# Kernel tuning notes

Measured on AMD Instinct MI355X. Metric: run time of the kernel, lower is better.

Reference implementation:

```python
import jax, jax.numpy as jnp
import numpy as np

SUB_NO = 20
T_NO = 201
E_NO = 2000
I_NO = 500
T_DATA = 20000

def _make_cden():
    C = np.zeros((SUB_NO, SUB_NO), dtype=np.float32)
    for i in range(SUB_NO):
        for c in (2 * i + 1, 2 * i + 2):
            if c < SUB_NO:
                C[i, c] = 1.0
    return C

C_DEN = _make_cden()
CHILDREN = [np.where(C_DEN[s] == 1)[0] for s in range(SUB_NO)]  # static tree structure


def setup_inputs() -> dict:
    key = jax.random.key(0)
    ks = jax.random.split(key, 12)
    eps = 1e-6
    inp = {}
    inp['S_e'] = jax.random.uniform(ks[0], (T_DATA, E_NO), dtype=jnp.float32)
    inp['S_i'] = jax.random.uniform(ks[1], (T_DATA, I_NO), dtype=jnp.float32)
    # uniform noise for REBAR reparam; clipped away from {0,1} so log(-log(u)) is finite
    inp['u'] = jnp.clip(jax.random.uniform(ks[2], (SUB_NO, E_NO + I_NO), dtype=jnp.float32), eps, 1.0 - eps)
    inp['v'] = jnp.clip(jax.random.uniform(ks[3], (SUB_NO, E_NO + I_NO), dtype=jnp.float32), eps, 1.0 - eps)
    inp['W_syn'] = jax.random.normal(ks[4], (SUB_NO, 2), dtype=jnp.float32) * 0.1
    inp['Tau_syn'] = jnp.ones((SUB_NO, 2), dtype=jnp.float32)
    inp['Delta_syn'] = jax.random.uniform(ks[5], (SUB_NO, 2), dtype=jnp.float32)
    inp['W_sub'] = jax.random.uniform(ks[6], (SUB_NO,), dtype=jnp.float32)
    inp['V_o'] = jax.random.normal(ks[7], (1,), dtype=jnp.float32)
    inp['Theta'] = jnp.zeros((SUB_NO,), dtype=jnp.float32)
    inp['C_syn_log'] = jnp.ones((SUB_NO, E_NO + I_NO), dtype=jnp.float32)
    return inp


def _H(x):
    # one-hot of per-column argmax (first max, as torch.argmax)
    idx = jnp.argmax(x, axis=0)
    return jax.nn.one_hot(idx, x.shape[0], axis=0, dtype=x.dtype)


def _reparam_pz(u, theta):
    return jnp.log(theta) - jnp.log(-jnp.log(u))


def _reparam_pz_b(v, b, theta):
    # b is one-hot per column; v_k = v at the b==1 row of each column
    v_k = jnp.sum(v * b, axis=0, keepdims=True)  # [1, cols]
    z_same = -jnp.log(-jnp.log(v))
    z_diff = -jnp.log(-jnp.log(v) / theta - jnp.log(v_k))
    return b * z_same + (1.0 - b) * z_diff


def _evaluate_f(C_syn, S_e, S_i, W_syn, Tau_syn, Delta_syn, W_sub, V_o):
    T_data = S_e.shape[0]
    C_syn_e = C_syn[:, :E_NO]          # [sub, E]
    C_syn_i = C_syn[:, -I_NO:]         # [sub, I]
    # double-exponential (alpha) synaptic kernels, vectorized over subunits & e/i
    t_raw = jnp.arange(T_NO, dtype=S_e.dtype)                               # [T_no]
    t = jnp.maximum(t_raw[None, None, :] - jnp.exp(Delta_syn)[:, :, None], 0.0)  # [sub,2,T_no]
    t_tau = t / jnp.exp(Tau_syn)[:, :, None]
    kern = t_tau * jnp.exp(-t_tau) * W_syn[:, :, None]                      # [sub,2,T_no]
    # project spikes onto subunits
    in_e = S_e @ C_syn_e.T   # [T, sub]
    in_i = S_i @ C_syn_i.T   # [T, sub]
    # causal depthwise conv: syn[t,s] = sum_tau kern[s,:,tau] * in[t-tau,s]
    inp = jnp.stack([in_e.T, in_i.T], axis=1).reshape(1, SUB_NO * 2, T_data)   # NCH
    k = jnp.flip(kern, axis=-1).reshape(SUB_NO * 2, 1, T_NO)                   # OIH
    filt = jax.lax.conv_general_dilated(
        inp, k, window_strides=(1,), padding=[(T_NO - 1, 0)],
        feature_group_count=SUB_NO * 2,
        dimension_numbers=('NCH', 'OIH', 'NCH'))
    syn_in = filt.reshape(SUB_NO, 2, T_data).sum(axis=1).T   # [T, sub]
    # tree-recurrent tanh aggregation (children have higher index than parents)
    sub_out = [None] * SUB_NO
    for s in range(SUB_NO):
        idx = SUB_NO - 1 - s
        ch = CHILDREN[idx]
        if ch.size == 0:
            sub_out[idx] = jnp.tanh(syn_in[:, idx])
        else:
            leaf = sum(sub_out[c] * W_sub[c] for c in ch)
            sub_out[idx] = jnp.tanh(syn_in[:, idx] + leaf)
    return sub_out[0] * W_sub[0] + V_o[0]


def reference(S_e, S_i, u, v, W_syn, Tau_syn, Delta_syn, W_sub, V_o, Theta, C_syn_log):
    theta = jax.nn.softmax(C_syn_log, axis=0)
    rebar_z = _reparam_pz(u, theta)
    hard_z = _H(rebar_z)
    rebar_zb = _reparam_pz_b(v, hard_z, theta)
    soft_z = jax.nn.sigmoid(rebar_z / 0.5) + 1e-9
    soft_zb = jax.nn.sigmoid(rebar_zb / 0.5) + 1e-9
    V_hard_z = _evaluate_f(hard_z, S_e, S_i, W_syn, Tau_syn, Delta_syn, W_sub, V_o)
    V_soft_z = _evaluate_f(soft_z, S_e, S_i, W_syn, Tau_syn, Delta_syn, W_sub, V_o)
    V_soft_zb = _evaluate_f(soft_zb, S_e, S_i, W_syn, Tau_syn, Delta_syn, W_sub, V_o)
    return (V_hard_z, V_soft_z, V_soft_zb, theta, hard_z, soft_z, soft_zb)
```

## Files before the change

kernel.cpp:

```cpp
#include <hip/hip_runtime.h>
#include <math.h>

#define SUBS 20
#define TAPS 201
#define ENO 2000
#define INO 500
#define TDATA 20000

typedef __bf16 bf16x8 __attribute__((ext_vector_type(8)));
typedef float f32x4 __attribute__((ext_vector_type(4)));

#define WGE_STRIDE 2048
#define WGI_STRIDE 512

#define WGE_OFF  0ull
#define WGI_OFF  262144ull
#define KERN_OFF 327680ull
#define INE_OFF  360448ull
#define INI_OFF  (INE_OFF + 4800000ull)
#define SYN_OFF  (INI_OFF + 4800000ull)

__device__ __forceinline__ unsigned short f2bf(float f) {
  union { float f; unsigned int u; } c; c.f = f;
  unsigned int u = c.u;
  return (unsigned short)((u + 0x7FFFu + ((u >> 16) & 1u)) >> 16);
}

__global__ __launch_bounds__(256) void prep_kernel(
    const float* __restrict__ u, const float* __restrict__ v,
    const float* __restrict__ C_log, const float* __restrict__ W_syn,
    const float* __restrict__ Tau_syn, const float* __restrict__ Delta_syn,
    float* __restrict__ out,
    unsigned short* __restrict__ wge, unsigned short* __restrict__ wgi,
    float* __restrict__ kern)
{
  if (blockIdx.x < 10) {
    const int n = blockIdx.x * 256 + threadIdx.x;
    if (n >= 2500) return;
    float x[SUBS], theta[SUBS], rebar[SUBS];
    float mx = -1e30f;
#pragma unroll
    for (int s = 0; s < SUBS; ++s) { x[s] = C_log[s*2500 + n]; mx = fmaxf(mx, x[s]); }
    float sum = 0.f;
#pragma unroll
    for (int s = 0; s < SUBS; ++s) { theta[s] = expf(x[s] - mx); sum += theta[s]; }
    const float inv = 1.f / sum;
    int idx = 0; float best = -1e30f;
#pragma unroll
    for (int s = 0; s < SUBS; ++s) {
      theta[s] *= inv;
      out[60000 + s*2500 + n] = theta[s];
      const float uu = u[s*2500 + n];
      const float r = logf(theta[s]) - logf(-logf(uu));
      rebar[s] = r;
      if (r > best) { best = r; idx = s; }
    }
    const float lvk = logf(v[idx*2500 + n]);
#pragma unroll
    for (int s = 0; s < SUBS; ++s) {
      const float hz = (s == idx) ? 1.f : 0.f;
      const float sz = 1.f / (1.f + expf(-2.f * rebar[s])) + 1e-9f;
      const float vv = v[s*2500 + n];
      const float zb = (s == idx) ? (-logf(-logf(vv)))
                                  : (-logf(-logf(vv) / theta[s] - lvk));
      const float szb = 1.f / (1.f + expf(-2.f * zb)) + 1e-9f;
      out[110000 + s*2500 + n] = hz;
      out[160000 + s*2500 + n] = sz;
      out[210000 + s*2500 + n] = szb;
      if (n < ENO) {
        wge[(s     )*WGE_STRIDE + n] = f2bf(hz);
        wge[(20 + s)*WGE_STRIDE + n] = f2bf(sz);
        wge[(40 + s)*WGE_STRIDE + n] = f2bf(szb);
      } else {
        const int k = n - ENO;
        wgi[(s     )*WGI_STRIDE + k] = f2bf(hz);
        wgi[(20 + s)*WGI_STRIDE + k] = f2bf(sz);
        wgi[(40 + s)*WGI_STRIDE + k] = f2bf(szb);
      }
    }
  } else {
    const int tid = threadIdx.x;
    for (int i = tid; i < 40*TAPS; i += 256) {
      const int ch = i / TAPS, m = i - ch*TAPS;
      const float dl  = expf(Delta_syn[ch]);
      const float tau = expf(Tau_syn[ch]);
      const float t  = fmaxf((float)m - dl, 0.f);
      const float tt = t / tau;
      kern[i] = tt * expf(-tt) * W_syn[ch];
    }
    for (int i = tid; i < 4*2048; i += 256) wge[(60 + (i >> 11))*WGE_STRIDE + (i & 2047)] = 0;
    for (int i = tid; i < 60*48;  i += 256) wge[(i / 48)*WGE_STRIDE + 2000 + (i % 48)] = 0;
    for (int i = tid; i < 4*512;  i += 256) wgi[(60 + (i >> 9))*WGI_STRIDE + (i & 511)] = 0;
    for (int i = tid; i < 60*12;  i += 256) wgi[(i / 12)*WGI_STRIDE + 500 + (i % 12)] = 0;
  }
}

__global__ __launch_bounds__(256) void gemm_kernel(
    const float* __restrict__ S_e, const float* __restrict__ S_i,
    const unsigned short* __restrict__ wge, const unsigned short* __restrict__ wgi,
    float* __restrict__ in_e, float* __restrict__ in_i)
{
  __shared__ unsigned short Alds[64*40];
  __shared__ unsigned short Blds[64*40];
  __shared__ float Cbuf[64*68];
  const int tid  = threadIdx.x;
  const int t0   = blockIdx.x * 64;
  const int wave = tid >> 6;
  const int lane = tid & 63;
  const int m16  = lane & 15;
  const int quad = lane >> 4;
  const int slotA = tid & 7;
  const int rowA  = tid >> 3;
  const int cB    = tid >> 2;
  const int slotB = tid & 3;

  for (int phase = 0; phase < 2; ++phase) {
    const float* S = phase ? S_i : S_e;
    const unsigned short* Wg = phase ? wgi : wge;
    float* outp = phase ? in_i : in_e;
    const int K       = phase ? INO : ENO;
    const int Wstride = phase ? WGI_STRIDE : WGE_STRIDE;
    const int steps   = phase ? 16 : 63;

    f32x4 acc0 = {0.f,0.f,0.f,0.f};
    f32x4 acc1 = acc0, acc2 = acc0, acc3 = acc0;

    for (int st = 0; st < steps; ++st) {
      const int k0 = st * 32;
#pragma unroll
      for (int p = 0; p < 2; ++p) {
        const int r = rowA + p*32;
        const int t = t0 + r;
        const int k = k0 + slotA*4;
        float4 val = make_float4(0.f, 0.f, 0.f, 0.f);
        if (t < TDATA) {
          if (k + 4 <= K) {
            val = *(const float4*)(S + (size_t)t*K + k);
          } else {
            val.x = (k+0 < K) ? S[(size_t)t*K + k+0] : 0.f;
            val.y = (k+1 < K) ? S[(size_t)t*K + k+1] : 0.f;
            val.z = (k+2 < K) ? S[(size_t)t*K + k+2] : 0.f;
            val.w = (k+3 < K) ? S[(size_t)t*K + k+3] : 0.f;
          }
        }
        unsigned short* dst = &Alds[r*40 + slotA*4];
        dst[0] = f2bf(val.x); dst[1] = f2bf(val.y);
        dst[2] = f2bf(val.z); dst[3] = f2bf(val.w);
      }
      *(uint4*)(&Blds[cB*40 + slotB*8]) =
          *(const uint4*)(Wg + (size_t)cB*Wstride + k0 + slotB*8);
      __syncthreads();
      const bf16x8 a  = *(const bf16x8*)(&Alds[(wave*16 + m16)*40 + quad*8]);
      const bf16x8 b0 = *(const bf16x8*)(&Blds[(      m16)*40 + quad*8]);
      const bf16x8 b1 = *(const bf16x8*)(&Blds[(16 + m16)*40 + quad*8]);
      const bf16x8 b2 = *(const bf16x8*)(&Blds[(32 + m16)*40 + quad*8]);
      const bf16x8 b3 = *(const bf16x8*)(&Blds[(48 + m16)*40 + quad*8]);
      acc0 = __builtin_amdgcn_mfma_f32_16x16x32_bf16(a, b0, acc0, 0, 0, 0);
      acc1 = __builtin_amdgcn_mfma_f32_16x16x32_bf16(a, b1, acc1, 0, 0, 0);
      acc2 = __builtin_amdgcn_mfma_f32_16x16x32_bf16(a, b2, acc2, 0, 0, 0);
      acc3 = __builtin_amdgcn_mfma_f32_16x16x32_bf16(a, b3, acc3, 0, 0, 0);
      __syncthreads();
    }
    const int rloc = wave*16 + quad*4;
#pragma unroll
    for (int r = 0; r < 4; ++r) {
      Cbuf[(      m16)*68 + rloc + r] = acc0[r];
      Cbuf[(16 + m16)*68 + rloc + r] = acc1[r];
      Cbuf[(32 + m16)*68 + rloc + r] = acc2[r];
      Cbuf[(48 + m16)*68 + rloc + r] = acc3[r];
    }
    __syncthreads();
    if (cB < 60) {
#pragma unroll
      for (int g = 0; g < 4; ++g) {
        const int tl = slotB*16 + g*4;
        const int t = t0 + tl;
        if (t < TDATA)
          *(float4*)(outp + (size_t)cB*TDATA + t) = *(const float4*)(&Cbuf[cB*68 + tl]);
      }
    }
    __syncthreads();
  }
}

__device__ __forceinline__ int swz(int i) { return i + (i >> 5); }

__global__ __launch_bounds__(256) void conv_kernel(
    const float* __restrict__ in_e, const float* __restrict__ in_i,
    const float* __restrict__ kern, float* __restrict__ syn)
{
  __shared__ float Ee[2320];
  __shared__ float Ei[2320];
  const int ch = blockIdx.y;
  const int t0 = blockIdx.x * 2048;
  const int s  = ch % SUBS;
  const float* pe = in_e + (size_t)ch * TDATA;
  const float* pi = in_i + (size_t)ch * TDATA;
  for (int i = threadIdx.x; i < 2248; i += 256) {
    const int g = t0 - 200 + i;
    const bool ok = (g >= 0) && (g < TDATA);
    Ee[swz(i)] = ok ? pe[g] : 0.f;
    Ei[swz(i)] = ok ? pi[g] : 0.f;
  }
  __syncthreads();
  const float* ke = kern + (size_t)(s*2    ) * TAPS;
  const float* ki = kern + (size_t)(s*2 + 1) * TAPS;
  const int tb = threadIdx.x * 8;
  float acc[8] = {0.f,0.f,0.f,0.f,0.f,0.f,0.f,0.f};
  float we[8], wi[8];
#pragma unroll
  for (int j = 0; j < 8; ++j) {
    we[j] = Ee[swz(tb + 200 + j)];
    wi[j] = Ei[swz(tb + 200 + j)];
  }
#pragma unroll 8
  for (int m = 0; m < TAPS; ++m) {
    const float k0 = ke[m];
    const float k1 = ki[m];
#pragma unroll
    for (int j = 0; j < 8; ++j)
      acc[j] = fmaf(we[j], k0, fmaf(wi[j], k1, acc[j]));
    if (m < TAPS - 1) {
#pragma unroll
      for (int j = 7; j > 0; --j) { we[j] = we[j-1]; wi[j] = wi[j-1]; }
      we[0] = Ee[swz(tb + 199 - m)];
      wi[0] = Ei[swz(tb + 199 - m)];
    }
  }
  const int t = t0 + tb;
  if (t < TDATA) {
    float* o = syn + (size_t)ch * TDATA + t;
    *(float4*)(o    ) = make_float4(acc[0], acc[1], acc[2], acc[3]);
    *(float4*)(o + 4) = make_float4(acc[4], acc[5], acc[6], acc[7]);
  }
}

__global__ __launch_bounds__(256) void tree_kernel(
    const float* __restrict__ syn, const float* __restrict__ W_sub,
    const float* __restrict__ V_o, float* __restrict__ out)
{
  const int t = blockIdx.x * 256 + threadIdx.x;
  const int var = blockIdx.y;
  if (t >= TDATA) return;
  const float* sp = syn + (size_t)var * SUBS * TDATA + t;
  float so[SUBS];
#pragma unroll
  for (int s = SUBS - 1; s >= 0; --s) {
    float val = sp[(size_t)s * TDATA];
    const int c1 = 2*s + 1, c2 = 2*s + 2;
    if (c1 < SUBS) val += so[c1] * W_sub[c1];
    if (c2 < SUBS) val += so[c2] * W_sub[c2];
    so[s] = tanhf(val);
  }
  out[(size_t)var * TDATA + t] = so[0] * W_sub[0] + V_o[0];
}

extern "C" void kernel_launch(void* const* d_in, const int* in_sizes, int n_in,
                              void* d_out, int out_size, void* d_ws, size_t ws_size,
                              hipStream_t stream) {
  const float* S_e     = (const float*)d_in[0];
  const float* S_i     = (const float*)d_in[1];
  const float* u       = (const float*)d_in[2];
  const float* v       = (const float*)d_in[3];
  const float* W_syn   = (const float*)d_in[4];
  const float* Tau_syn = (const float*)d_in[5];
  const float* Delta   = (const float*)d_in[6];
  const float* W_sub   = (const float*)d_in[7];
  const float* V_o     = (const float*)d_in[8];
  const float* C_log   = (const float*)d_in[10];
  float* out = (float*)d_out;
  char* ws = (char*)d_ws;
  unsigned short* wge = (unsigned short*)(ws + WGE_OFF);
  unsigned short* wgi = (unsigned short*)(ws + WGI_OFF);
  float* kern = (float*)(ws + KERN_OFF);
  float* in_e = (float*)(ws + INE_OFF);
  float* in_i = (float*)(ws + INI_OFF);
  float* syn  = (float*)(ws + SYN_OFF);

  prep_kernel<<<dim3(11), dim3(256), 0, stream>>>(u, v, C_log, W_syn, Tau_syn,
                                                  Delta, out, wge, wgi, kern);
  gemm_kernel<<<dim3(313), dim3(256), 0, stream>>>(S_e, S_i, wge, wgi, in_e, in_i);
  conv_kernel<<<dim3(10, 60), dim3(256), 0, stream>>>(in_e, in_i, kern, syn);
  tree_kernel<<<dim3(79, 3), dim3(256), 0, stream>>>(syn, W_sub, V_o, out);
}
```

Measured before the change: 397.1 us.

## Split GEMM K dimension across blocks with atomic accumulation for more parallelism

The GEMM grid grows from 313 blocks to 313x5: the E-phase K=2000 is split into four 512-wide chunks whose partial sums are combined with atomicAdd, and the I-phase runs as its own chunk. Before, each block ran both phases one after the other. The E output buffer is now zeroed by extra blocks in the prep kernel, and the A/B/C LDS tiles share one union. The aim is to fill the GPU's many CUs instead of running about one block per CU with a long serial K loop. The cost is 4x atomic traffic on in_e, a zeroing pass over 9.6 MB, scalar strided output stores, and non-deterministic float summation order.

Result: slower. 580.0 us (+46.1%).

```diff
diff --git a/kernel.cpp b/kernel.cpp
--- a/kernel.cpp
+++ b/kernel.cpp
@@ -20,6 +20,8 @@
 #define INI_OFF  (INE_OFF + 4800000ull)
 #define SYN_OFF  (INI_OFF + 4800000ull)
 
+#define ZERO_BLOCKS 117
+
 __device__ __forceinline__ unsigned short f2bf(float f) {
   union { float f; unsigned int u; } c; c.f = f;
   unsigned int u = c.u;
@@ -32,7 +34,7 @@
     const float* __restrict__ Tau_syn, const float* __restrict__ Delta_syn,
     float* __restrict__ out,
     unsigned short* __restrict__ wge, unsigned short* __restrict__ wgi,
-    float* __restrict__ kern)
+    float* __restrict__ kern, float* __restrict__ in_e)
 {
   if (blockIdx.x < 10) {
     const int n = blockIdx.x * 256 + threadIdx.x;
@@ -78,7 +80,7 @@
         wgi[(40 + s)*WGI_STRIDE + k] = f2bf(szb);
       }
     }
-  } else {
+  } else if (blockIdx.x == 10) {
     const int tid = threadIdx.x;
     for (int i = tid; i < 40*TAPS; i += 256) {
       const int ch = i / TAPS, m = i - ch*TAPS;
@@ -92,6 +94,12 @@
     for (int i = tid; i < 60*48;  i += 256) wge[(i / 48)*WGE_STRIDE + 2000 + (i % 48)] = 0;
     for (int i = tid; i < 4*512;  i += 256) wgi[(60 + (i >> 9))*WGI_STRIDE + (i & 511)] = 0;
     for (int i = tid; i < 60*12;  i += 256) wgi[(i / 12)*WGI_STRIDE + 500 + (i % 12)] = 0;
+  } else {
+    const int zb = blockIdx.x - 11;
+    const int total4 = (2 * 60 * TDATA) / 4;
+    const float4 z = make_float4(0.f, 0.f, 0.f, 0.f);
+    for (int i = zb*256 + threadIdx.x; i < total4; i += ZERO_BLOCKS*256)
+      ((float4*)in_e)[i] = z;
   }
 }
 
@@ -100,11 +108,14 @@
     const unsigned short* __restrict__ wge, const unsigned short* __restrict__ wgi,
     float* __restrict__ in_e, float* __restrict__ in_i)
 {
-  __shared__ unsigned short Alds[64*40];
-  __shared__ unsigned short Blds[64*40];
-  __shared__ float Cbuf[64*68];
+  __shared__ union {
+    struct { unsigned short A[64*40]; unsigned short B[64*40]; } s;
+    float C[64*67];
+  } lds;
   const int tid  = threadIdx.x;
   const int t0   = blockIdx.x * 64;
+  const int chunk = blockIdx.y;
+  const bool isE = (chunk < 4);
   const int wave = tid >> 6;
   const int lane = tid & 63;
   const int m16  = lane & 15;
@@ -114,72 +125,76 @@
   const int cB    = tid >> 2;
   const int slotB = tid & 3;
 
-  for (int phase = 0; phase < 2; ++phase) {
-    const float* S = phase ? S_i : S_e;
-    const unsigned short* Wg = phase ? wgi : wge;
-    float* outp = phase ? in_i : in_e;
-    const int K       = phase ? INO : ENO;
-    const int Wstride = phase ? WGI_STRIDE : WGE_STRIDE;
-    const int steps   = phase ? 16 : 63;
-
-    f32x4 acc0 = {0.f,0.f,0.f,0.f};
-    f32x4 acc1 = acc0, acc2 = acc0, acc3 = acc0;
-
-    for (int st = 0; st < steps; ++st) {
-      const int k0 = st * 32;
-#pragma unroll
-      for (int p = 0; p < 2; ++p) {
-        const int r = rowA + p*32;
-        const int t = t0 + r;
-        const int k = k0 + slotA*4;
-        float4 val = make_float4(0.f, 0.f, 0.f, 0.f);
-        if (t < TDATA) {
-          if (k + 4 <= K) {
-            val = *(const float4*)(S + (size_t)t*K + k);
-          } else {
-            val.x = (k+0 < K) ? S[(size_t)t*K + k+0] : 0.f;
-            val.y = (k+1 < K) ? S[(size_t)t*K + k+1] : 0.f;
-            val.z = (k+2 < K) ? S[(size_t)t*K + k+2] : 0.f;
-            val.w = (k+3 < K) ? S[(size_t)t*K + k+3] : 0.f;
-          }
+  const float* S = isE ? S_e : S_i;
+  const unsigned short* Wg = isE ? wgi : wgi;
+  Wg = isE ? wge : wgi;
+  float* outp = isE ? in_e : in_i;
+  const int K       = isE ? ENO : INO;
+  const int Wstride = isE ? WGE_STRIDE : WGI_STRIDE;
+  const int k_base  = isE ? chunk * 512 : 0;
+  const int steps   = (chunk == 3) ? 15 : 16;
+
+  f32x4 acc0 = {0.f,0.f,0.f,0.f};
+  f32x4 acc1 = acc0, acc2 = acc0, acc3 = acc0;
+
+  for (int st = 0; st < steps; ++st) {
+    const int k0 = k_base + st * 32;
+#pragma unroll
+    for (int p = 0; p < 2; ++p) {
+      const int r = rowA + p*32;
+      const int t = t0 + r;
+      const int k = k0 + slotA*4;
+      float4 val = make_float4(0.f, 0.f, 0.f, 0.f);
+      if (t < TDATA) {
+        if (k + 4 <= K) {
+          val = *(const float4*)(S + (size_t)t*K + k);
+        } else {
+          val.x = (k+0 < K) ? S[(size_t)t*K + k+0] : 0.f;
+          val.y = (k+1 < K) ? S[(size_t)t*K + k+1] : 0.f;
+          val.z = (k+2 < K) ? S[(size_t)t*K + k+2] : 0.f;
+          val.w = (k+3 < K) ? S[(size_t)t*K + k+3] : 0.f;
         }
-        unsigned short* dst = &Alds[r*40 + slotA*4];
-        dst[0] = f2bf(val.x); dst[1] = f2bf(val.y);
-        dst[2] = f2bf(val.z); dst[3] = f2bf(val.w);
       }
-      *(uint4*)(&Blds[cB*40 + slotB*8]) =
-          *(const uint4*)(Wg + (size_t)cB*Wstride + k0 + slotB*8);
-      __syncthreads();
-      const bf16x8 a  = *(const bf16x8*)(&Alds[(wave*16 + m16)*40 + quad*8]);
-      const bf16x8 b0 = *(const bf16x8*)(&Blds[(      m16)*40 + quad*8]);
-      const bf16x8 b1 = *(const bf16x8*)(&Blds[(16 + m16)*40 + quad*8]);
-      const bf16x8 b2 = *(const bf16x8*)(&Blds[(32 + m16)*40 + quad*8]);
-      const bf16x8 b3 = *(const bf16x8*)(&Blds[(48 + m16)*40 + quad*8]);
-      acc0 = __builtin_amdgcn_mfma_f32_16x16x32_bf16(a, b0, acc0, 0, 0, 0);
-      acc1 = __builtin_amdgcn_mfma_f32_16x16x32_bf16(a, b1, acc1, 0, 0, 0);
-      acc2 = __builtin_amdgcn_mfma_f32_16x16x32_bf16(a, b2, acc2, 0, 0, 0);
-      acc3 = __builtin_amdgcn_mfma_f32_16x16x32_bf16(a, b3, acc3, 0, 0, 0);
-      __syncthreads();
-    }
-    const int rloc = wave*16 + quad*4;
-#pragma unroll
-    for (int r = 0; r < 4; ++r) {
-      Cbuf[(      m16)*68 + rloc + r] = acc0[r];
-      Cbuf[(16 + m16)*68 + rloc + r] = acc1[r];
-      Cbuf[(32 + m16)*68 + rloc + r] = acc2[r];
-      Cbuf[(48 + m16)*68 + rloc + r] = acc3[r];
-    }
+      ushort4 w4;
+      w4.x = f2bf(val.x); w4.y = f2bf(val.y);
+      w4.z = f2bf(val.z); w4.w = f2bf(val.w);
+      *(ushort4*)(&lds.s.A[r*40 + slotA*4]) = w4;
+    }
+    *(uint4*)(&lds.s.B[cB*40 + slotB*8]) =
+        *(const uint4*)(Wg + (size_t)cB*Wstride + k0 + slotB*8);
     __syncthreads();
-    if (cB < 60) {
-#pragma unroll
-      for (int g = 0; g < 4; ++g) {
-        const int tl = slotB*16 + g*4;
-        const int t = t0 + tl;
-        if (t < TDATA)
-          *(float4*)(outp + (size_t)cB*TDATA + t) = *(const float4*)(&Cbuf[cB*68 + tl]);
+    const bf16x8 a  = *(const bf16x8*)(&lds.s.A[(wave*16 + m16)*40 + quad*8]);
+    const bf16x8 b0 = *(const bf16x8*)(&lds.s.B[(      m16)*40 + quad*8]);
+    const bf16x8 b1 = *(const bf16x8*)(&lds.s.B[(16 + m16)*40 + quad*8]);
+    const bf16x8 b2 = *(const bf16x8*)(&lds.s.B[(32 + m16)*40 + quad*8]);
+    const bf16x8 b3 = *(const bf16x8*)(&lds.s.B[(48 + m16)*40 + quad*8]);
+    acc0 = __builtin_amdgcn_mfma_f32_16x16x32_bf16(a, b0, acc0, 0, 0, 0);
+    acc1 = __builtin_amdgcn_mfma_f32_16x16x32_bf16(a, b1, acc1, 0, 0, 0);
+    acc2 = __builtin_amdgcn_mfma_f32_16x16x32_bf16(a, b2, acc2, 0, 0, 0);
+    acc3 = __builtin_amdgcn_mfma_f32_16x16x32_bf16(a, b3, acc3, 0, 0, 0);
+    __syncthreads();
+  }
+  const int rloc = wave*16 + quad*4;
+#pragma unroll
+  for (int r = 0; r < 4; ++r) {
+    lds.C[(      m16)*67 + rloc + r] = acc0[r];
+    lds.C[(16 + m16)*67 + rloc + r] = acc1[r];
+    lds.C[(32 + m16)*67 + rloc + r] = acc2[r];
+    lds.C[(48 + m16)*67 + rloc + r] = acc3[r];
+  }
+  __syncthreads();
+  if (cB < 60) {
+    float* o = outp + (size_t)cB * TDATA;
+#pragma unroll
+    for (int g = 0; g < 16; ++g) {
+      const int tl = slotB*16 + g;
+      const int t = t0 + tl;
+      if (t < TDATA) {
+        const float val = lds.C[cB*67 + tl];
+        if (isE) atomicAdd(o + t, val);
+        else     o[t] = val;
       }
     }
-    __syncthreads();
   }
 }
 
@@ -277,9 +292,9 @@
   float* in_i = (float*)(ws + INI_OFF);
   float* syn  = (float*)(ws + SYN_OFF);
 
-  prep_kernel<<<dim3(11), dim3(256), 0, stream>>>(u, v, C_log, W_syn, Tau_syn,
-                                                  Delta, out, wge, wgi, kern);
-  gemm_kernel<<<dim3(313), dim3(256), 0, stream>>>(S_e, S_i, wge, wgi, in_e, in_i);
+  prep_kernel<<<dim3(11 + ZERO_BLOCKS), dim3(256), 0, stream>>>(
+      u, v, C_log, W_syn, Tau_syn, Delta, out, wge, wgi, kern, in_e);
+  gemm_kernel<<<dim3(313, 5), dim3(256), 0, stream>>>(S_e, S_i, wge, wgi, in_e, in_i);
   conv_kernel<<<dim3(10, 60), dim3(256), 0, stream>>>(in_e, in_i, kern, syn);
   tree_kernel<<<dim3(79, 3), dim3(256), 0, stream>>>(syn, W_sub, V_o, out);
 }
```

## Split GEMM K dimension across a 2D grid and add partial-sum reduction

Applied to the files above, without the earlier changes.

The GEMM grid becomes (313,3): the excitatory K range is split across two chunks and the inhibitory input gets its own chunk, which raises the block count from 313 to 939 to improve CU occupancy on a 256-CU GPU. The second excitatory chunk writes partial sums into the syn workspace, and a new reduce kernel adds them into in_e before the convolution. Accumulators are now stored straight from MFMA registers to global memory instead of being transposed through an LDS C buffer. The A-tile LDS store is vectorized as a ushort4. The cost is an extra kernel launch plus an extra read/write pass over the 60xT partial buffer, and the direct stores are less coalesced.

Result: faster. 343.6 us (-13.5%).

```diff
diff --git a/kernel.cpp b/kernel.cpp
--- a/kernel.cpp
+++ b/kernel.cpp
@@ -98,13 +98,14 @@
 __global__ __launch_bounds__(256) void gemm_kernel(
     const float* __restrict__ S_e, const float* __restrict__ S_i,
     const unsigned short* __restrict__ wge, const unsigned short* __restrict__ wgi,
-    float* __restrict__ in_e, float* __restrict__ in_i)
+    float* __restrict__ in_e, float* __restrict__ in_i, float* __restrict__ part)
 {
   __shared__ unsigned short Alds[64*40];
   __shared__ unsigned short Blds[64*40];
-  __shared__ float Cbuf[64*68];
   const int tid  = threadIdx.x;
   const int t0   = blockIdx.x * 64;
+  const int chunk = blockIdx.y;
+  const bool isE = (chunk < 2);
   const int wave = tid >> 6;
   const int lane = tid & 63;
   const int m16  = lane & 15;
@@ -114,72 +115,75 @@
   const int cB    = tid >> 2;
   const int slotB = tid & 3;
 
-  for (int phase = 0; phase < 2; ++phase) {
-    const float* S = phase ? S_i : S_e;
-    const unsigned short* Wg = phase ? wgi : wge;
-    float* outp = phase ? in_i : in_e;
-    const int K       = phase ? INO : ENO;
-    const int Wstride = phase ? WGI_STRIDE : WGE_STRIDE;
-    const int steps   = phase ? 16 : 63;
-
-    f32x4 acc0 = {0.f,0.f,0.f,0.f};
-    f32x4 acc1 = acc0, acc2 = acc0, acc3 = acc0;
-
-    for (int st = 0; st < steps; ++st) {
-      const int k0 = st * 32;
-#pragma unroll
-      for (int p = 0; p < 2; ++p) {
-        const int r = rowA + p*32;
-        const int t = t0 + r;
-        const int k = k0 + slotA*4;
-        float4 val = make_float4(0.f, 0.f, 0.f, 0.f);
-        if (t < TDATA) {
-          if (k + 4 <= K) {
-            val = *(const float4*)(S + (size_t)t*K + k);
-          } else {
-            val.x = (k+0 < K) ? S[(size_t)t*K + k+0] : 0.f;
-            val.y = (k+1 < K) ? S[(size_t)t*K + k+1] : 0.f;
-            val.z = (k+2 < K) ? S[(size_t)t*K + k+2] : 0.f;
-            val.w = (k+3 < K) ? S[(size_t)t*K + k+3] : 0.f;
-          }
+  const float* S = isE ? S_e : S_i;
+  const unsigned short* Wg = isE ? wge : wgi;
+  float* outp = (chunk == 0) ? in_e : ((chunk == 1) ? part : in_i);
+  const int K       = isE ? ENO : INO;
+  const int Wstride = isE ? WGE_STRIDE : WGI_STRIDE;
+  const int k_base  = (chunk == 1) ? 1024 : 0;
+  const int steps   = (chunk == 0) ? 32 : ((chunk == 1) ? 31 : 16);
+
+  f32x4 acc0 = {0.f,0.f,0.f,0.f};
+  f32x4 acc1 = acc0, acc2 = acc0, acc3 = acc0;
+
+  for (int st = 0; st < steps; ++st) {
+    const int k0 = k_base + st * 32;
+#pragma unroll
+    for (int p = 0; p < 2; ++p) {
+      const int r = rowA + p*32;
+      const int t = t0 + r;
+      const int k = k0 + slotA*4;
+      float4 val = make_float4(0.f, 0.f, 0.f, 0.f);
+      if (t < TDATA) {
+        if (k + 4 <= K) {
+          val = *(const float4*)(S + (size_t)t*K + k);
+        } else {
+          val.x = (k+0 < K) ? S[(size_t)t*K + k+0] : 0.f;
+          val.y = (k+1 < K) ? S[(size_t)t*K + k+1] : 0.f;
+          val.z = (k+2 < K) ? S[(size_t)t*K + k+2] : 0.f;
+          val.w = (k+3 < K) ? S[(size_t)t*K + k+3] : 0.f;
         }
-        unsigned short* dst = &Alds[r*40 + slotA*4];
-        dst[0] = f2bf(val.x); dst[1] = f2bf(val.y);
-        dst[2] = f2bf(val.z); dst[3] = f2bf(val.w);
       }
-      *(uint4*)(&Blds[cB*40 + slotB*8]) =
-          *(const uint4*)(Wg + (size_t)cB*Wstride + k0 + slotB*8);
-      __syncthreads();
-      const bf16x8 a  = *(const bf16x8*)(&Alds[(wave*16 + m16)*40 + quad*8]);
-      const bf16x8 b0 = *(const bf16x8*)(&Blds[(      m16)*40 + quad*8]);
-      const bf16x8 b1 = *(const bf16x8*)(&Blds[(16 + m16)*40 + quad*8]);
-      const bf16x8 b2 = *(const bf16x8*)(&Blds[(32 + m16)*40 + quad*8]);
-      const bf16x8 b3 = *(const bf16x8*)(&Blds[(48 + m16)*40 + quad*8]);
-      acc0 = __builtin_amdgcn_mfma_f32_16x16x32_bf16(a, b0, acc0, 0, 0, 0);
-      acc1 = __builtin_amdgcn_mfma_f32_16x16x32_bf16(a, b1, acc1, 0, 0, 0);
-      acc2 = __builtin_amdgcn_mfma_f32_16x16x32_bf16(a, b2, acc2, 0, 0, 0);
-      acc3 = __builtin_amdgcn_mfma_f32_16x16x32_bf16(a, b3, acc3, 0, 0, 0);
-      __syncthreads();
-    }
-    const int rloc = wave*16 + quad*4;
-#pragma unroll
-    for (int r = 0; r < 4; ++r) {
-      Cbuf[(      m16)*68 + rloc + r] = acc0[r];
-      Cbuf[(16 + m16)*68 + rloc + r] = acc1[r];
-      Cbuf[(32 + m16)*68 + rloc + r] = acc2[r];
-      Cbuf[(48 + m16)*68 + rloc + r] = acc3[r];
-    }
+      ushort4 w4;
+      w4.x = f2bf(val.x); w4.y = f2bf(val.y);
+      w4.z = f2bf(val.z); w4.w = f2bf(val.w);
+      *(ushort4*)(&Alds[r*40 + slotA*4]) = w4;
+    }
+    *(uint4*)(&Blds[cB*40 + slotB*8]) =
+        *(const uint4*)(Wg + (size_t)cB*Wstride + k0 + slotB*8);
     __syncthreads();
-    if (cB < 60) {
-#pragma unroll
-      for (int g = 0; g < 4; ++g) {
-        const int tl = slotB*16 + g*4;
-        const int t = t0 + tl;
-        if (t < TDATA)
-          *(float4*)(outp + (size_t)cB*TDATA + t) = *(const float4*)(&Cbuf[cB*68 + tl]);
-      }
-    }
+    const bf16x8 a  = *(const bf16x8*)(&Alds[(wave*16 + m16)*40 + quad*8]);
+    const bf16x8 b0 = *(const bf16x8*)(&Blds[(      m16)*40 + quad*8]);
+    const bf16x8 b1 = *(const bf16x8*)(&Blds[(16 + m16)*40 + quad*8]);
+    const bf16x8 b2 = *(const bf16x8*)(&Blds[(32 + m16)*40 + quad*8]);
+    const bf16x8 b3 = *(const bf16x8*)(&Blds[(48 + m16)*40 + quad*8]);
+    acc0 = __builtin_amdgcn_mfma_f32_16x16x32_bf16(a, b0, acc0, 0, 0, 0);
+    acc1 = __builtin_amdgcn_mfma_f32_16x16x32_bf16(a, b1, acc1, 0, 0, 0);
+    acc2 = __builtin_amdgcn_mfma_f32_16x16x32_bf16(a, b2, acc2, 0, 0, 0);
+    acc3 = __builtin_amdgcn_mfma_f32_16x16x32_bf16(a, b3, acc3, 0, 0, 0);
     __syncthreads();
+  }
+  const int t = t0 + wave*16 + quad*4;
+  if (t < TDATA) {
+    float* o = outp + t;
+    *(float4*)(o + (size_t)(     m16)*TDATA) = *(float4*)&acc0;
+    *(float4*)(o + (size_t)(16 + m16)*TDATA) = *(float4*)&acc1;
+    *(float4*)(o + (size_t)(32 + m16)*TDATA) = *(float4*)&acc2;
+    if (m16 < 12)
+      *(float4*)(o + (size_t)(48 + m16)*TDATA) = *(float4*)&acc3;
+  }
+}
+
+__global__ __launch_bounds__(256) void reduce_kernel(
+    float* __restrict__ in_e, const float* __restrict__ part)
+{
+  const int i = blockIdx.x * 256 + threadIdx.x;
+  const int n4 = 60 * TDATA / 4;
+  if (i < n4) {
+    float4 a = ((const float4*)in_e)[i];
+    const float4 p = ((const float4*)part)[i];
+    a.x += p.x; a.y += p.y; a.z += p.z; a.w += p.w;
+    ((float4*)in_e)[i] = a;
   }
 }
 
@@ -279,7 +283,9 @@
 
   prep_kernel<<<dim3(11), dim3(256), 0, stream>>>(u, v, C_log, W_syn, Tau_syn,
                                                   Delta, out, wge, wgi, kern);
-  gemm_kernel<<<dim3(313), dim3(256), 0, stream>>>(S_e, S_i, wge, wgi, in_e, in_i);
+  gemm_kernel<<<dim3(313, 3), dim3(256), 0, stream>>>(S_e, S_i, wge, wgi,
+                                                      in_e, in_i, syn);
+  reduce_kernel<<<dim3(1172), dim3(256), 0, stream>>>(in_e, syn);
   conv_kernel<<<dim3(10, 60), dim3(256), 0, stream>>>(in_e, in_i, kern, syn);
   tree_kernel<<<dim3(79, 3), dim3(256), 0, stream>>>(syn, W_sub, V_o, out);
 }
```
